# Kernel tuning notes

Hardware: AMD Instinct MI355X
Metric: run time of the kernel (lower is better)

The kernel has to match this reference:

```python
import jax, jax.numpy as jnp
import numpy as np

B, T, D = 4, 2048, 1024
H = 16
DH = D // H

def setup_inputs() -> dict:
    key = jax.random.key(0)
    k1, k2, k3 = jax.random.split(key, 3)
    x = jax.random.normal(k1, (B, T, D), dtype=jnp.float32)
    causal_mask = jnp.tril(jnp.ones((T, T), dtype=bool))[None, None]  # (1,1,T,T)
    Wqkv = jax.random.normal(k2, (D, 3 * D), dtype=jnp.float32) * (1.0 / np.sqrt(D))
    Wout = jax.random.normal(k3, (D, D), dtype=jnp.float32) * (1.0 / np.sqrt(D))
    return {"x": x, "causal_mask": causal_mask, "Wqkv": Wqkv, "Wout": Wout}

def reference(x, causal_mask, Wqkv, Wout):
    Bb, Tt, C = x.shape
    scale = jnp.sqrt(jnp.asarray(DH, dtype=x.dtype))
    qkv = x @ Wqkv                                   # (B,T,3D)
    qkv = qkv.reshape(Bb, Tt, 3, H, DH)
    qkv = jnp.transpose(qkv, (2, 0, 3, 1, 4))        # (3,B,H,T,DH)
    q, k, v = qkv[0], qkv[1], qkv[2]
    attn = jnp.einsum('bhqd,bhkd->bhqk', q, k) / scale
    attn = jnp.where(causal_mask, attn, jnp.asarray(-jnp.inf, dtype=attn.dtype))
    attn = jax.nn.softmax(attn, axis=-1)             # dropout p=0 -> identity
    out = jnp.einsum('bhqk,bhkd->bhqd', attn, v)     # (B,H,T,DH)
    out = jnp.transpose(out, (0, 2, 1, 3)).reshape(Bb, Tt, C)
    return out @ Wout
```

## Files before the change

### kernel.cpp

```cpp
#include <hip/hip_runtime.h>
#include <hip/hip_bf16.h>
#include <math.h>


#define Bb 4
#define Tt 2048
#define Dd 1024
#define Hh 16
#define DH 64
#define Mrows (Bb*Tt)
#define NEGBIG (-1.0e30f)
#define KB64 (Dd/64)
#define CHUNKS 1024
#define TILEU16 8192

typedef unsigned short u16;
typedef __attribute__((ext_vector_type(8))) short bf16x8;
typedef __attribute__((ext_vector_type(4))) float f32x4;
typedef __attribute__((ext_vector_type(4))) unsigned int u32x4;

__device__ __forceinline__ u16 f2bf(float f) {
    union { float f; unsigned int i; } v; v.f = f;
    unsigned int x = v.i;
    return (u16)((x + 0x7fffu + ((x >> 16) & 1u)) >> 16);
}

__device__ __forceinline__ unsigned int cvt_pk_bf16(float lo, float hi) {
    unsigned int r;
    asm("v_cvt_pk_bf16_f32 %0, %1, %2" : "=v"(r) : "v"(lo), "v"(hi));
    return r;
}

__device__ __forceinline__ void perm32swap(unsigned& x, unsigned& y) {
    asm("v_permlane32_swap_b32 %0, %1" : "+v"(x), "+v"(y));
}
__device__ __forceinline__ void perm16swap(unsigned& x, unsigned& y) {
    asm("v_permlane16_swap_b32 %0, %1" : "+v"(x), "+v"(y));
}

__device__ __forceinline__ float exp2_(float x) {
#if __has_builtin(__builtin_amdgcn_exp2f)
    return __builtin_amdgcn_exp2f(x);
#else
    return __expf(x * 0.69314718056f);
#endif
}

typedef __attribute__((address_space(1))) const void glob_cv;
typedef __attribute__((address_space(3))) void lds_v;
__device__ __forceinline__ void gl2lds16(const void* g, void* l) {
    __builtin_amdgcn_global_load_lds((glob_cv*)g, (lds_v*)l, 16, 0, 0);
}

__device__ __forceinline__ void conv_w_body(const float* __restrict__ W,
                                            u16* __restrict__ Wt, int N,
                                            int nb, int kb, int tid,
                                            u16 (*t)[68]) {
    const int k0 = kb * 64, n0 = nb * 128;
    const int k = tid >> 2, ng = tid & 3;
    const float* s = W + (size_t)(k0 + k) * N + n0 + ng * 32;
    #pragma unroll
    for (int i = 0; i < 8; ++i) {
        float4 f = *(const float4*)(s + i * 4);
        const int n = ng * 32 + i * 4;
        t[n + 0][k] = f2bf(f.x); t[n + 1][k] = f2bf(f.y);
        t[n + 2][k] = f2bf(f.z); t[n + 3][k] = f2bf(f.w);
    }
    __syncthreads();
    u16* base = Wt + (size_t)(nb * KB64 + kb) * TILEU16;
    #pragma unroll
    for (int it = 0; it < 4; ++it) {
        const int c = it * 256 + tid;
        const int row = c & 127, kq = c >> 7;
        union { u16 u[8]; uint4 v; } o;
        #pragma unroll
        for (int j = 0; j < 8; ++j) o.u[j] = t[row][kq * 8 + j];
        *(uint4*)(base + (size_t)c * 8) = o.v;
    }
}

__global__ __launch_bounds__(256) void convert_all(const float* __restrict__ x,
                                                   const float* __restrict__ Wqkv,
                                                   const float* __restrict__ Wout,
                                                   u16* __restrict__ xT,
                                                   u16* __restrict__ WqkvT,
                                                   u16* __restrict__ WoutT) {
    __shared__ u16 t[128][68];
    const int bid = blockIdx.x, tid = threadIdx.x;
    if (bid < 1024) {
        const int mb = bid >> 4, kb = bid & 15;
        const int row = tid & 127, half = tid >> 7;
        const float* s = x + (size_t)(mb * 128 + row) * Dd + kb * 64 + half * 32;
        u16* base = xT + (size_t)bid * TILEU16;
        #pragma unroll
        for (int cq = 0; cq < 4; ++cq) {
            const int kq = half * 4 + cq;
            float4 f0 = *(const float4*)(s + cq * 8);
            float4 f1 = *(const float4*)(s + cq * 8 + 4);
            uint4 o;
            o.x = cvt_pk_bf16(f0.x, f0.y); o.y = cvt_pk_bf16(f0.z, f0.w);
            o.z = cvt_pk_bf16(f1.x, f1.y); o.w = cvt_pk_bf16(f1.z, f1.w);
            *(uint4*)(base + (size_t)(kq * 128 + row) * 8) = o;
        }
    } else if (bid < 1408) {
        const int r = bid - 1024;
        conv_w_body(Wqkv, WqkvT, 3 * Dd, r % 24, r / 24, tid, t);
    } else {
        const int r = bid - 1408;
        conv_w_body(Wout, WoutT, Dd, r % 8, r / 8, tid, t);
    }
}

template <int MODE>
__global__ __launch_bounds__(512, 2) void gemm_mfma(const u16* __restrict__ At,
                                                    const u16* __restrict__ Bt,
                                                    u16* __restrict__ Qo,
                                                    u16* __restrict__ KT,
                                                    u16* __restrict__ VtT,
                                                    float* __restrict__ Out) {
    __shared__ u16 As[3][2][8 * 128 * 8];
    __shared__ u16 Bs[3][8 * 128 * 8];

    const int tid  = threadIdx.x;
    const int lane = tid & 63, w = tid >> 6;
    const int ml   = lane & 15, q = lane >> 4;
    const int wm   = w >> 1, wn = w & 1;
    const int mh   = wm >> 1;
    const int mrow = (wm & 1) * 64;

    const int nbx = gridDim.x;
    const int nwg = nbx * gridDim.y;
    int id = blockIdx.y * nbx + blockIdx.x;
    id = (id & 7) * (nwg >> 3) + (id >> 3);
    const int bxs = id % nbx, bys = id / nbx;

    const u16* A0 = At + (size_t)(2 * bys)     * KB64 * TILEU16;
    const u16* A1 = At + (size_t)(2 * bys + 1) * KB64 * TILEU16;
    const u16* B0 = Bt + (size_t)bxs           * KB64 * TILEU16;

    f32x4 acc[4][4];
    #pragma unroll
    for (int i = 0; i < 4; ++i)
        #pragma unroll
        for (int j = 0; j < 4; ++j) acc[i][j] = (f32x4){0.f, 0.f, 0.f, 0.f};

    #define STAGE_A(k_, sl_, it_) do {                                        \
        const int c_ = (it_) * 512 + tid;                                     \
        const int h_ = c_ >> 10, cc_ = c_ & 1023;                             \
        gl2lds16((h_ ? A1 : A0) + (size_t)(k_) * TILEU16 + (size_t)cc_ * 8,   \
                 (char*)As[sl_][h_] + (size_t)cc_ * 16);                      \
    } while (0)
    #define STAGE_B(k_, sl_, it_) do {                                        \
        const int c_ = (it_) * 512 + tid;                                     \
        gl2lds16(B0 + (size_t)(k_) * TILEU16 + (size_t)c_ * 8,                \
                 (char*)Bs[sl_] + (size_t)c_ * 16);                           \
    } while (0)

    STAGE_A(0, 0, 0); STAGE_A(0, 0, 1); STAGE_A(0, 0, 2); STAGE_A(0, 0, 3);
    STAGE_B(0, 0, 0); STAGE_B(0, 0, 1);
    STAGE_A(1, 1, 0); STAGE_A(1, 1, 1); STAGE_A(1, 1, 2); STAGE_A(1, 1, 3);
    STAGE_B(1, 1, 0); STAGE_B(1, 1, 1);

    for (int k = 0; k < KB64; ++k) {
        const int sl = k % 3;
        if (k == KB64 - 1) asm volatile("s_waitcnt vmcnt(0)" ::: "memory");
        else               asm volatile("s_waitcnt vmcnt(6)" ::: "memory");
        __builtin_amdgcn_s_barrier();

        const int k2 = k + 2, s2 = k2 % 3;

        bf16x8 bfr[4][2], af0[2][2];
        #pragma unroll
        for (int ks = 0; ks < 2; ++ks) {
            const int kq = ks * 4 + q;
            #pragma unroll
            for (int j = 0; j < 4; ++j)
                bfr[j][ks] = *(const bf16x8*)((const char*)Bs[sl] +
                        ((kq * 128) + wn * 64 + j * 16 + ml) * 16);
            #pragma unroll
            for (int i = 0; i < 2; ++i)
                af0[i][ks] = *(const bf16x8*)((const char*)As[sl][mh] +
                        ((kq * 128) + mrow + i * 16 + ml) * 16);
        }
        if (k2 < KB64) { STAGE_A(k2, s2, 0); STAGE_A(k2, s2, 1); STAGE_B(k2, s2, 0); }

        __builtin_amdgcn_s_setprio(1);
        #pragma unroll
        for (int i = 0; i < 2; ++i)
            #pragma unroll
            for (int j = 0; j < 4; ++j)
                #pragma unroll
                for (int ks = 0; ks < 2; ++ks)
                    acc[i][j] = __builtin_amdgcn_mfma_f32_16x16x32_bf16(
                            bfr[j][ks], af0[i][ks], acc[i][j], 0, 0, 0);
        __builtin_amdgcn_s_setprio(0);

        __builtin_amdgcn_s_barrier();

        bf16x8 af1[2][2];
        #pragma unroll
        for (int ks = 0; ks < 2; ++ks) {
            const int kq = ks * 4 + q;
            #pragma unroll
            for (int i = 0; i < 2; ++i)
                af1[i][ks] = *(const bf16x8*)((const char*)As[sl][mh] +
                        ((kq * 128) + mrow + (i + 2) * 16 + ml) * 16);
        }
        if (k2 < KB64) { STAGE_A(k2, s2, 2); STAGE_A(k2, s2, 3); STAGE_B(k2, s2, 1); }

        __builtin_amdgcn_s_setprio(1);
        #pragma unroll
        for (int i = 0; i < 2; ++i)
            #pragma unroll
            for (int j = 0; j < 4; ++j)
                #pragma unroll
                for (int ks = 0; ks < 2; ++ks)
                    acc[i + 2][j] = __builtin_amdgcn_mfma_f32_16x16x32_bf16(
                            bfr[j][ks], af1[i][ks], acc[i + 2][j], 0, 0, 0);
        __builtin_amdgcn_s_setprio(0);
    }
    #undef STAGE_A
    #undef STAGE_B

    if (MODE == 0) {
        const int s  = (bxs * 128) >> 10;
        const int h0 = ((bxs * 128) & 1023) >> 6;
        #pragma unroll
        for (int i = 0; i < 4; ++i) {
            const int m  = bys * 256 + wm * 64 + i * 16 + ml;
            const int bb = m >> 11, t = m & 2047;
            const int bhn = bb * Hh + h0 + wn;
            #pragma unroll
            for (int j = 0; j < 4; ++j) {
                const int dh = j * 16 + q * 4;
                if (s == 2) {
                    u16* vb = VtT + (size_t)(bhn * 16 + (t >> 7)) * TILEU16;
                    #pragma unroll
                    for (int r = 0; r < 4; ++r)
                        vb[(size_t)(((t >> 3) & 15) * 64 + dh + r) * 8 + (t & 7)]
                            = f2bf(acc[i][j][r]);
                } else if (s == 1) {
                    uint2 pk;
                    pk.x = cvt_pk_bf16(acc[i][j][0], acc[i][j][1]);
                    pk.y = cvt_pk_bf16(acc[i][j][2], acc[i][j][3]);
                    *(uint2*)(KT + (size_t)(bhn * 16 + (t >> 7)) * TILEU16 +
                              (size_t)((j * 2 + (q >> 1)) * 128 + (t & 127)) * 8 +
                              (q & 1) * 4) = pk;
                } else {
                    const float sc = 0.125f * 1.44269504089f;
                    uint2 pk;
                    pk.x = cvt_pk_bf16(acc[i][j][0] * sc, acc[i][j][1] * sc);
                    pk.y = cvt_pk_bf16(acc[i][j][2] * sc, acc[i][j][3] * sc);
                    *(uint2*)(Qo + ((size_t)bhn * Tt + t) * DH + dh) = pk;
                }
            }
        }
    } else {
        #pragma unroll
        for (int i = 0; i < 4; ++i) {
            const int m = bys * 256 + wm * 64 + i * 16 + ml;
            #pragma unroll
            for (int j = 0; j < 4; ++j) {
                const int n = bxs * 128 + wn * 64 + j * 16 + q * 4;
                float4 st = {acc[i][j][0], acc[i][j][1], acc[i][j][2], acc[i][j][3]};
                *(float4*)(Out + (size_t)m * Dd + n) = st;
            }
        }
    }
}

__device__ __forceinline__ void softmax_pack(f32x4 (&st)[8], float& l_i,
                                             unsigned (&d)[8], unsigned (&e)[8],
                                             int q, int qrow, bool diag) {
    if (diag) {
        #pragma unroll
        for (int kt = 0; kt < 8; ++kt)
            #pragma unroll
            for (int r = 0; r < 4; ++r)
                if (kt * 16 + q * 4 + r > qrow) st[kt][r] = NEGBIG;
    }
    float rs = 0.f;
    #pragma unroll
    for (int kt = 0; kt < 8; ++kt) {
        const float p0 = exp2_(st[kt][0]);
        const float p1 = exp2_(st[kt][1]);
        const float p2 = exp2_(st[kt][2]);
        const float p3 = exp2_(st[kt][3]);
        rs += (p0 + p1) + (p2 + p3);
        d[kt] = cvt_pk_bf16(p0, p1);
        e[kt] = cvt_pk_bf16(p2, p3);
    }
    rs += __shfl_xor(rs, 16, 64);
    rs += __shfl_xor(rs, 32, 64);
    l_i += rs;
}

__device__ __forceinline__ bf16x8 build_bp(const unsigned (&d)[8],
                                           const unsigned (&e)[8], int s) {
    unsigned w0 = d[2 * s], w2 = d[2 * s + 1];
    perm32swap(w0, w2); perm16swap(w0, w2);
    unsigned w1 = e[2 * s], w3 = e[2 * s + 1];
    perm32swap(w1, w3); perm16swap(w1, w3);
    union { u32x4 u; bf16x8 b; } cv;
    cv.u = (u32x4){w0, w1, w2, w3};
    return cv.b;
}

__global__ __launch_bounds__(256, 3) void attn_mfma(const u16* __restrict__ Q,
                                                    const u16* __restrict__ KT,
                                                    const u16* __restrict__ VtT,
                                                    u16* __restrict__ AOT) {
    __shared__ u16 Ks[8 * 128 * 8];
    __shared__ u16 Vs[2][16 * 64 * 8];

    const int tid  = threadIdx.x;
    const int lane = tid & 63, w = tid >> 6;
    const int nl   = lane & 15, q = lane >> 4;

    int id = blockIdx.y * 8 + blockIdx.x;
    id = (id & 7) * 64 + (id >> 3);
    const int bxp = id & 7, bh = id >> 3;
    const int b = bh >> 4, h = bh & 15;
    const size_t kbase = (size_t)bh * Tt * DH;

    for (int phase = 0; phase < 2; ++phase) {
        const int qt = phase ? (15 - bxp) : bxp;
        const int q0 = qt * 128;
        const int nj = qt + 1;

        bf16x8 qf[2][2];
        #pragma unroll
        for (int qb = 0; qb < 2; ++qb)
            #pragma unroll
            for (int s = 0; s < 2; ++s)
                qf[qb][s] = *(const bf16x8*)(Q + kbase +
                        (size_t)(q0 + w * 32 + qb * 16 + nl) * DH + (s * 4 + q) * 8);

        float l_i[2] = {0.f, 0.f};
        f32x4 accO[2][4];
        #pragma unroll
        for (int qb = 0; qb < 2; ++qb)
            #pragma unroll
            for (int dt = 0; dt < 4; ++dt) accO[qb][dt] = (f32x4){0.f, 0.f, 0.f, 0.f};

        __syncthreads();
        {
            const u16* Kb = KT  + (size_t)(bh * 16) * TILEU16;
            const u16* Vb = VtT + (size_t)(bh * 16) * TILEU16;
            #pragma unroll
            for (int it = 0; it < 4; ++it) {
                const int c = it * 256 + tid;
                gl2lds16(Kb + (size_t)c * 8, (char*)Ks + c * 16);
                gl2lds16(Vb + (size_t)c * 8, (char*)Vs[0] + c * 16);
            }
        }

        for (int jt = 0; jt < nj; ++jt) {
            const int buf = jt & 1;
            __syncthreads();

            f32x4 st0[8], st1[8];
            #pragma unroll
            for (int kt = 0; kt < 8; ++kt) {
                st0[kt] = (f32x4){0.f, 0.f, 0.f, 0.f};
                st1[kt] = (f32x4){0.f, 0.f, 0.f, 0.f};
            }
            __builtin_amdgcn_s_setprio(1);
            #pragma unroll
            for (int s = 0; s < 2; ++s) {
                #pragma unroll
                for (int kt = 0; kt < 8; ++kt) {
                    bf16x8 ak = *(const bf16x8*)((const char*)Ks +
                            ((s * 4 + q) * 128 + kt * 16 + nl) * 16);
                    st0[kt] = __builtin_amdgcn_mfma_f32_16x16x32_bf16(
                            ak, qf[0][s], st0[kt], 0, 0, 0);
                    st1[kt] = __builtin_amdgcn_mfma_f32_16x16x32_bf16(
                            ak, qf[1][s], st1[kt], 0, 0, 0);
                }
            }
            __builtin_amdgcn_s_setprio(0);

            __syncthreads();

            if (jt + 1 < nj) {
                const u16* Kb = KT  + (size_t)(bh * 16 + jt + 1) * TILEU16;
                const u16* Vb = VtT + (size_t)(bh * 16 + jt + 1) * TILEU16;
                #pragma unroll
                for (int it = 0; it < 4; ++it) {
                    const int c = it * 256 + tid;
                    gl2lds16(Kb + (size_t)c * 8, (char*)Ks + c * 16);
                    gl2lds16(Vb + (size_t)c * 8, (char*)Vs[buf ^ 1] + c * 16);
                }
            }

            const bool diag = (jt == nj - 1);
            unsigned d0[8], e0[8], d1[8], e1[8];
            softmax_pack(st0, l_i[0], d0, e0, q, w * 32 + nl, diag);
            softmax_pack(st1, l_i[1], d1, e1, q, w * 32 + 16 + nl, diag);

            __builtin_amdgcn_s_setprio(1);
            #pragma unroll
            for (int s = 0; s < 4; ++s) {
                bf16x8 bp0 = build_bp(d0, e0, s);
                bf16x8 bp1 = build_bp(d1, e1, s);
                #pragma unroll
                for (int dt = 0; dt < 4; ++dt) {
                    bf16x8 av = *(const bf16x8*)((const char*)Vs[buf] +
                            ((s * 4 + q) * 64 + dt * 16 + nl) * 16);
                    accO[0][dt] = __builtin_amdgcn_mfma_f32_16x16x32_bf16(
                            av, bp0, accO[0][dt], 0, 0, 0);
                    accO[1][dt] = __builtin_amdgcn_mfma_f32_16x16x32_bf16(
                            av, bp1, accO[1][dt], 0, 0, 0);
                }
            }
            __builtin_amdgcn_s_setprio(0);
        }

        #pragma unroll
        for (int qb = 0; qb < 2; ++qb) {
            const float inv = 1.0f / l_i[qb];
            const int t = q0 + w * 32 + qb * 16 + nl;
            const int m = b * Tt + t;
            u16* ab = AOT + (size_t)((m >> 7) * KB64 + h) * TILEU16;
            #pragma unroll
            for (int dt = 0; dt < 4; ++dt) {
                uint2 pk;
                pk.x = cvt_pk_bf16(accO[qb][dt][0] * inv, accO[qb][dt][1] * inv);
                pk.y = cvt_pk_bf16(accO[qb][dt][2] * inv, accO[qb][dt][3] * inv);
                *(uint2*)(ab + (size_t)((dt * 2 + (q >> 1)) * 128 + (m & 127)) * 8 +
                          (q & 1) * 4) = pk;
            }
        }
    }
}

extern "C" void kernel_launch(void* const* d_in, const int* in_sizes, int n_in,
                              void* d_out, int out_size, void* d_ws, size_t ws_size,
                              hipStream_t stream) {
    const float* x_raw    = (const float*)d_in[0];
    const float* Wqkv_raw = (const float*)d_in[2];
    const float* Wout_raw = (const float*)d_in[3];
    float* out = (float*)d_out;

    const size_t SZ = (size_t)Bb * Hh * Tt * DH;
    u16* ws = (u16*)d_ws;
    u16* Qw     = ws;
    u16* KT     = ws + SZ;
    u16* VtT    = ws + 2 * SZ;
    u16* AOT    = ws + 3 * SZ;
    u16* WqkvT  = ws + 4 * SZ;
    u16* WoutT  = WqkvT + (size_t)3 * Dd * Dd;
    u16* xT     = (u16*)d_out;

    convert_all<<<dim3(1536), 256, 0, stream>>>(x_raw, Wqkv_raw, Wout_raw,
                                                xT, WqkvT, WoutT);
    gemm_mfma<0><<<dim3(3 * Dd / 128, Mrows / 256), 512, 0, stream>>>(xT, WqkvT, Qw, KT, VtT, nullptr);
    attn_mfma  <<<dim3(Tt / 256, Bb * Hh), 256, 0, stream>>>(Qw, KT, VtT, AOT);
    gemm_mfma<1><<<dim3(Dd / 128, Mrows / 256), 512, 0, stream>>>(AOT, WoutT, nullptr, nullptr, nullptr, out);
}
```

Measured before the change: 236.6 us.

## Halve GEMM K-step to 32 and raise occupancy to four workgroups per CU

```diff
diff --git a/kernel.cpp b/kernel.cpp
--- a/kernel.cpp
+++ b/kernel.cpp
@@ -11,6 +11,7 @@
 #define Mrows (Bb*Tt)
 #define NEGBIG (-1.0e30f)
 #define KB64 (Dd/64)
+#define KB32 (Dd/32)
 #define CHUNKS 1024
 #define TILEU16 8192
 
@@ -112,14 +113,14 @@
 }
 
 template <int MODE>
-__global__ __launch_bounds__(512, 2) void gemm_mfma(const u16* __restrict__ At,
+__global__ __launch_bounds__(512, 4) void gemm_mfma(const u16* __restrict__ At,
                                                     const u16* __restrict__ Bt,
                                                     u16* __restrict__ Qo,
                                                     u16* __restrict__ KT,
                                                     u16* __restrict__ VtT,
                                                     float* __restrict__ Out) {
-    __shared__ u16 As[3][2][8 * 128 * 8];
-    __shared__ u16 Bs[3][8 * 128 * 8];
+    __shared__ u16 As[3][2][4 * 128 * 8];
+    __shared__ u16 Bs[3][4 * 128 * 8];
 
     const int tid  = threadIdx.x;
     const int lane = tid & 63, w = tid >> 6;
@@ -144,83 +145,52 @@
         #pragma unroll
         for (int j = 0; j < 4; ++j) acc[i][j] = (f32x4){0.f, 0.f, 0.f, 0.f};
 
-    #define STAGE_A(k_, sl_, it_) do {                                        \
-        const int c_ = (it_) * 512 + tid;                                     \
-        const int h_ = c_ >> 10, cc_ = c_ & 1023;                             \
-        gl2lds16((h_ ? A1 : A0) + (size_t)(k_) * TILEU16 + (size_t)cc_ * 8,   \
+    #define STAGE_A32(k_, sl_, it_) do {                                      \
+        const int c_ = (it_) * 512 + tid;                        \
+        const int h_ = c_ >> 9, cc_ = c_ & 511;                               \
+        gl2lds16((h_ ? A1 : A0) + (size_t)((k_) >> 1) * TILEU16 +             \
+                 ((k_) & 1) * 4096 + (size_t)cc_ * 8,                         \
                  (char*)As[sl_][h_] + (size_t)cc_ * 16);                      \
     } while (0)
-    #define STAGE_B(k_, sl_, it_) do {                                        \
-        const int c_ = (it_) * 512 + tid;                                     \
-        gl2lds16(B0 + (size_t)(k_) * TILEU16 + (size_t)c_ * 8,                \
-                 (char*)Bs[sl_] + (size_t)c_ * 16);                           \
+    #define STAGE_B32(k_, sl_) do {                                          \
+        gl2lds16(B0 + (size_t)((k_) >> 1) * TILEU16 +                         \
+                 ((k_) & 1) * 4096 + (size_t)tid * 8,                         \
+                 (char*)Bs[sl_] + (size_t)tid * 16);                          \
     } while (0)
 
-    STAGE_A(0, 0, 0); STAGE_A(0, 0, 1); STAGE_A(0, 0, 2); STAGE_A(0, 0, 3);
-    STAGE_B(0, 0, 0); STAGE_B(0, 0, 1);
-    STAGE_A(1, 1, 0); STAGE_A(1, 1, 1); STAGE_A(1, 1, 2); STAGE_A(1, 1, 3);
-    STAGE_B(1, 1, 0); STAGE_B(1, 1, 1);
-
-    for (int k = 0; k < KB64; ++k) {
+    STAGE_A32(0, 0, 0); STAGE_A32(0, 0, 1); STAGE_B32(0, 0);
+    STAGE_A32(1, 1, 0); STAGE_A32(1, 1, 1); STAGE_B32(1, 1);
+
+    for (int k = 0; k < KB32; ++k) {
         const int sl = k % 3;
-        if (k == KB64 - 1) asm volatile("s_waitcnt vmcnt(0)" ::: "memory");
-        else               asm volatile("s_waitcnt vmcnt(6)" ::: "memory");
+        if (k == KB32 - 1) asm volatile("s_waitcnt vmcnt(0)" ::: "memory");
+        else               asm volatile("s_waitcnt vmcnt(3)" ::: "memory");
         __builtin_amdgcn_s_barrier();
 
         const int k2 = k + 2, s2 = k2 % 3;
-
-        bf16x8 bfr[4][2], af0[2][2];
-        #pragma unroll
-        for (int ks = 0; ks < 2; ++ks) {
-            const int kq = ks * 4 + q;
+        if (k2 < KB32) { STAGE_A32(k2, s2, 0); STAGE_A32(k2, s2, 1); STAGE_B32(k2, s2); }
+
+        bf16x8 bfr[4], af[4];
+        #pragma unroll
+        for (int j = 0; j < 4; ++j)
+            bfr[j] = *(const bf16x8*)((const char*)Bs[sl] +
+                    ((q * 128) + wn * 64 + j * 16 + ml) * 16);
+        #pragma unroll
+        for (int i = 0; i < 4; ++i)
+            af[i] = *(const bf16x8*)((const char*)As[sl][mh] +
+                    ((q * 128) + mrow + i * 16 + ml) * 16);
+
+        __builtin_amdgcn_s_setprio(1);
+        #pragma unroll
+        for (int i = 0; i < 4; ++i)
             #pragma unroll
             for (int j = 0; j < 4; ++j)
-                bfr[j][ks] = *(const bf16x8*)((const char*)Bs[sl] +
-                        ((kq * 128) + wn * 64 + j * 16 + ml) * 16);
-            #pragma unroll
-            for (int i = 0; i < 2; ++i)
-                af0[i][ks] = *(const bf16x8*)((const char*)As[sl][mh] +
-                        ((kq * 128) + mrow + i * 16 + ml) * 16);
-        }
-        if (k2 < KB64) { STAGE_A(k2, s2, 0); STAGE_A(k2, s2, 1); STAGE_B(k2, s2, 0); }
-
-        __builtin_amdgcn_s_setprio(1);
-        #pragma unroll
-        for (int i = 0; i < 2; ++i)
-            #pragma unroll
-            for (int j = 0; j < 4; ++j)
-                #pragma unroll
-                for (int ks = 0; ks < 2; ++ks)
-                    acc[i][j] = __builtin_amdgcn_mfma_f32_16x16x32_bf16(
-                            bfr[j][ks], af0[i][ks], acc[i][j], 0, 0, 0);
+                acc[i][j] = __builtin_amdgcn_mfma_f32_16x16x32_bf16(
+                        bfr[j], af[i], acc[i][j], 0, 0, 0);
         __builtin_amdgcn_s_setprio(0);
-
-        __builtin_amdgcn_s_barrier();
-
-        bf16x8 af1[2][2];
-        #pragma unroll
-        for (int ks = 0; ks < 2; ++ks) {
-            const int kq = ks * 4 + q;
-            #pragma unroll
-            for (int i = 0; i < 2; ++i)
-                af1[i][ks] = *(const bf16x8*)((const char*)As[sl][mh] +
-                        ((kq * 128) + mrow + (i + 2) * 16 + ml) * 16);
-        }
-        if (k2 < KB64) { STAGE_A(k2, s2, 2); STAGE_A(k2, s2, 3); STAGE_B(k2, s2, 1); }
-
-        __builtin_amdgcn_s_setprio(1);
-        #pragma unroll
-        for (int i = 0; i < 2; ++i)
-            #pragma unroll
-            for (int j = 0; j < 4; ++j)
-                #pragma unroll
-                for (int ks = 0; ks < 2; ++ks)
-                    acc[i + 2][j] = __builtin_amdgcn_mfma_f32_16x16x32_bf16(
-                            bfr[j][ks], af1[i][ks], acc[i + 2][j], 0, 0, 0);
-        __builtin_amdgcn_s_setprio(0);
-    }
-    #undef STAGE_A
-    #undef STAGE_B
+    }
+    #undef STAGE_A32
+    #undef STAGE_B32
 
     if (MODE == 0) {
         const int s  = (bxs * 128) >> 10;
```

Result: slower. 260.1 us (+9.9%).
